# Kernel optimization log

Hardware: AMD Instinct MI355X
Metric: run time of the kernel (lower is better)

Reference implementation:

```python
import jax, jax.numpy as jnp
import numpy as np

ALPHA = 0.2  # Config.alpha, GAT default LeakyReLU slope
NUM_REL = 4
N = 4096          # num_e == batch of nodes
IN_F = 256
OUT_F = 64


def setup_inputs() -> dict:
    key = jax.random.key(0)
    k1, k2, k3, k4 = jax.random.split(key, 4)
    inp = jax.random.normal(k1, (N, IN_F), dtype=jnp.float32)
    adj = jax.random.uniform(k2, (N, N), dtype=jnp.float32)
    # xavier_uniform with gain=1.414 (sqrt(2))
    gain = 1.414
    limW = gain * np.sqrt(6.0 / (IN_F + OUT_F))
    W = jax.random.uniform(k3, (IN_F, OUT_F), minval=-limW, maxval=limW, dtype=jnp.float32)
    lima = gain * np.sqrt(6.0 / (2 * OUT_F + 1))
    a = jax.random.uniform(k4, (2 * OUT_F, 1), minval=-lima, maxval=lima, dtype=jnp.float32)
    return {"input": inp, "adj": adj, "W": W, "a": a}


def reference(input, adj, W, a):
    # h: (N, F_out)
    h = input @ W
    # The torch code builds an (N, N, 2F) concat tensor then matmuls with a.
    # Algebraically: e_ij = leakyrelu(h_i . a1 + h_j . a2) with a = [a1; a2].
    a1, a2 = a[:OUT_F], a[OUT_F:]            # (F,1) each
    s1 = (h @ a1)                            # (N,1) -> row term
    s2 = (h @ a2)                            # (N,1) -> col term
    e = jax.nn.leaky_relu(s1 + s2.T, negative_slope=ALPHA)  # (N,N)
    # attention = adj * e, replicated per relation, softmax over keys (dim 2)
    att = adj * e                            # (N,N)
    att = jnp.broadcast_to(att[None, :, :], (NUM_REL, N, N))
    att = jax.nn.softmax(att, axis=2)        # (R,N,N)
    # dropout is identity in eval mode
    h_prime = jnp.einsum('rij,jf->rif', att, h)  # (R,N,F_out)
    return jax.nn.elu(h_prime)               # concat=True -> elu
```

## Files before the change

### kernel.cpp

```cpp
#include <hip/hip_runtime.h>


#define NN 4096
#define INF 256
#define OUTF 64
#define ALPHA 0.2f
#define KCHUNKS 8
#define KCH (NN / KCHUNKS)

typedef __bf16 bf16;
typedef __bf16 bf16x4 __attribute__((ext_vector_type(4)));
typedef __bf16 bf16x8 __attribute__((ext_vector_type(8)));
typedef float floatx4 __attribute__((ext_vector_type(4)));

__global__ __launch_bounds__(256) void k_h(const float* __restrict__ input,
                                           const float* __restrict__ W,
                                           const float* __restrict__ a,
                                           bf16* __restrict__ hT,
                                           float* __restrict__ s1,
                                           float* __restrict__ s2) {
    const int wid  = threadIdx.x >> 6;
    const int lane = threadIdx.x & 63;
    const int row  = blockIdx.x * 4 + wid;
    const float* in_row = input + (size_t)row * INF;
    float acc = 0.f;
    #pragma unroll 8
    for (int k = 0; k < INF; ++k)
        acc = fmaf(in_row[k], W[k * OUTF + lane], acc);
    hT[(size_t)lane * NN + row] = (bf16)acc;
    float v1 = acc * a[lane];
    float v2 = acc * a[OUTF + lane];
    #pragma unroll
    for (int off = 32; off; off >>= 1) {
        v1 += __shfl_down(v1, off);
        v2 += __shfl_down(v2, off);
    }
    if (lane == 0) { s1[row] = v1; s2[row] = v2; }
}

__global__ __launch_bounds__(256) void k_p(const float* __restrict__ adj,
                                           const float* __restrict__ s1,
                                           const float* __restrict__ s2,
                                           bf16* __restrict__ P) {
    const int i = blockIdx.x;
    const int t = threadIdx.x;
    const int lane = t & 63, wid = t >> 6;
    const float s1i = s1[i];
    const float4* arow = (const float4*)(adj + (size_t)i * NN);
    const float4* s2v  = (const float4*)s2;
    float att[16];
    float m = -3.0e38f;
    #pragma unroll
    for (int it = 0; it < 4; ++it) {
        const int j4 = t + 256 * it;
        float4 av = arow[j4];
        float4 sv = s2v[j4];
        float e;
        e = s1i + sv.x; e = (e > 0.f ? e : ALPHA * e) * av.x; att[it*4+0] = e; m = fmaxf(m, e);
        e = s1i + sv.y; e = (e > 0.f ? e : ALPHA * e) * av.y; att[it*4+1] = e; m = fmaxf(m, e);
        e = s1i + sv.z; e = (e > 0.f ? e : ALPHA * e) * av.z; att[it*4+2] = e; m = fmaxf(m, e);
        e = s1i + sv.w; e = (e > 0.f ? e : ALPHA * e) * av.w; att[it*4+3] = e; m = fmaxf(m, e);
    }
    __shared__ float redmax[4], redsum[4];
    #pragma unroll
    for (int off = 32; off; off >>= 1) m = fmaxf(m, __shfl_xor(m, off));
    if (lane == 0) redmax[wid] = m;
    __syncthreads();
    m = fmaxf(fmaxf(redmax[0], redmax[1]), fmaxf(redmax[2], redmax[3]));
    float p[16];
    float lsum = 0.f;
    #pragma unroll
    for (int k = 0; k < 16; ++k) { p[k] = __expf(att[k] - m); lsum += p[k]; }
    #pragma unroll
    for (int off = 32; off; off >>= 1) lsum += __shfl_xor(lsum, off);
    if (lane == 0) redsum[wid] = lsum;
    __syncthreads();
    lsum = redsum[0] + redsum[1] + redsum[2] + redsum[3];
    const float rinv = 1.0f / lsum;
    bf16x4* prow = (bf16x4*)(P + (size_t)i * NN);
    #pragma unroll
    for (int it = 0; it < 4; ++it) {
        const int j4 = t + 256 * it;
        bf16x4 pv;
        pv[0] = (bf16)(p[it*4+0] * rinv);
        pv[1] = (bf16)(p[it*4+1] * rinv);
        pv[2] = (bf16)(p[it*4+2] * rinv);
        pv[3] = (bf16)(p[it*4+3] * rinv);
        prow[j4] = pv;
    }
}

__global__ __launch_bounds__(64) void k_g(const bf16* __restrict__ P,
                                          const bf16* __restrict__ hT,
                                          float* __restrict__ partial) {
    const int rg   = blockIdx.x;
    const int kc   = blockIdx.y;
    const int lane = threadIdx.x;
    const int r = lane & 15, q = lane >> 4;
    floatx4 acc[4] = {{0,0,0,0},{0,0,0,0},{0,0,0,0},{0,0,0,0}};
    const bf16* Abase = P + (size_t)(rg * 16 + r) * NN + kc * KCH + q * 8;
    const size_t hrow = (size_t)NN;
    const int kbase = kc * KCH + q * 8;
    #pragma unroll 4
    for (int s = 0; s < KCH / 32; ++s) {
        bf16x8 afrag = *(const bf16x8*)(Abase + s * 32);
        #pragma unroll
        for (int nt = 0; nt < 4; ++nt) {
            bf16x8 bfrag = *(const bf16x8*)(hT + (size_t)(nt * 16 + r) * hrow + kbase + s * 32);
            acc[nt] = __builtin_amdgcn_mfma_f32_16x16x32_bf16(afrag, bfrag, acc[nt], 0, 0, 0);
        }
    }
    float* pout = partial + (size_t)kc * (NN * OUTF);
    #pragma unroll
    for (int nt = 0; nt < 4; ++nt) {
        #pragma unroll
        for (int reg = 0; reg < 4; ++reg) {
            const int row = rg * 16 + q * 4 + reg;
            const int col = nt * 16 + r;
            pout[(size_t)row * OUTF + col] = acc[nt][reg];
        }
    }
}

__global__ __launch_bounds__(256) void k_e(const float* __restrict__ partial,
                                           float* __restrict__ out) {
    const int idx = blockIdx.x * 256 + threadIdx.x;
    float s = 0.f;
    #pragma unroll
    for (int c = 0; c < KCHUNKS; ++c) s += partial[(size_t)c * (NN * OUTF) + idx];
    const float r = s > 0.f ? s : (__expf(s) - 1.0f);
    #pragma unroll
    for (int rr = 0; rr < 4; ++rr) out[(size_t)rr * (NN * OUTF) + idx] = r;
}

extern "C" void kernel_launch(void* const* d_in, const int* in_sizes, int n_in,
                              void* d_out, int out_size, void* d_ws, size_t ws_size,
                              hipStream_t stream) {
    (void)in_sizes; (void)n_in; (void)out_size; (void)ws_size;
    const float* input = (const float*)d_in[0];
    const float* adj   = (const float*)d_in[1];
    const float* W     = (const float*)d_in[2];
    const float* a     = (const float*)d_in[3];
    float* out = (float*)d_out;

    char* ws = (char*)d_ws;
    bf16*  hT      = (bf16*)ws;
    float* s1      = (float*)(ws + (512 << 10));
    float* s2      = (float*)(ws + (528 << 10));
    bf16*  P       = (bf16*)(ws + (544 << 10));
    float* partial = (float*)(ws + (544 << 10) + (32u << 20));

    hipLaunchKernelGGL(k_h, dim3(NN / 4), dim3(256), 0, stream, input, W, a, hT, s1, s2);
    hipLaunchKernelGGL(k_p, dim3(NN), dim3(256), 0, stream, adj, s1, s2, P);
    hipLaunchKernelGGL(k_g, dim3(NN / 16, KCHUNKS), dim3(64), 0, stream, P, hT, partial);
    hipLaunchKernelGGL(k_e, dim3(NN * OUTF / 256), dim3(256), 0, stream, partial, out);
}
```

Measured before the change: 148.2 us.

## Fuse attention softmax, P@h MFMA and ELU epilogue into one kernel

```diff
diff --git a/kernel.cpp b/kernel.cpp
--- a/kernel.cpp
+++ b/kernel.cpp
@@ -5,11 +5,8 @@
 #define INF 256
 #define OUTF 64
 #define ALPHA 0.2f
-#define KCHUNKS 8
-#define KCH (NN / KCHUNKS)
 
 typedef __bf16 bf16;
-typedef __bf16 bf16x4 __attribute__((ext_vector_type(4)));
 typedef __bf16 bf16x8 __attribute__((ext_vector_type(8)));
 typedef float floatx4 __attribute__((ext_vector_type(4)));
 
@@ -38,99 +35,78 @@
     if (lane == 0) { s1[row] = v1; s2[row] = v2; }
 }
 
-__global__ __launch_bounds__(256) void k_p(const float* __restrict__ adj,
-                                           const float* __restrict__ s1,
-                                           const float* __restrict__ s2,
-                                           bf16* __restrict__ P) {
-    const int i = blockIdx.x;
-    const int t = threadIdx.x;
-    const int lane = t & 63, wid = t >> 6;
+__global__ __launch_bounds__(512, 1) void k_f(const float* __restrict__ adj,
+                                              const float* __restrict__ s1,
+                                              const float* __restrict__ s2,
+                                              const bf16* __restrict__ hT,
+                                              float* __restrict__ out) {
+    const int b    = blockIdx.x;
+    const int tid  = threadIdx.x;
+    const int w    = tid >> 6;
+    const int lane = tid & 63;
+    const int q = lane >> 4, r = lane & 15;
+    const int i = b * 16 + r;
+
     const float s1i = s1[i];
-    const float4* arow = (const float4*)(adj + (size_t)i * NN);
-    const float4* s2v  = (const float4*)s2;
-    float att[16];
-    float m = -3.0e38f;
-    #pragma unroll
-    for (int it = 0; it < 4; ++it) {
-        const int j4 = t + 256 * it;
-        float4 av = arow[j4];
-        float4 sv = s2v[j4];
-        float e;
-        e = s1i + sv.x; e = (e > 0.f ? e : ALPHA * e) * av.x; att[it*4+0] = e; m = fmaxf(m, e);
-        e = s1i + sv.y; e = (e > 0.f ? e : ALPHA * e) * av.y; att[it*4+1] = e; m = fmaxf(m, e);
-        e = s1i + sv.z; e = (e > 0.f ? e : ALPHA * e) * av.z; att[it*4+2] = e; m = fmaxf(m, e);
-        e = s1i + sv.w; e = (e > 0.f ? e : ALPHA * e) * av.w; att[it*4+3] = e; m = fmaxf(m, e);
-    }
-    __shared__ float redmax[4], redsum[4];
-    #pragma unroll
-    for (int off = 32; off; off >>= 1) m = fmaxf(m, __shfl_xor(m, off));
-    if (lane == 0) redmax[wid] = m;
-    __syncthreads();
-    m = fmaxf(fmaxf(redmax[0], redmax[1]), fmaxf(redmax[2], redmax[3]));
-    float p[16];
+    const float* arow = adj + (size_t)i * NN;
+
+    floatx4 acc[4] = {{0,0,0,0},{0,0,0,0},{0,0,0,0},{0,0,0,0}};
     float lsum = 0.f;
-    #pragma unroll
-    for (int k = 0; k < 16; ++k) { p[k] = __expf(att[k] - m); lsum += p[k]; }
-    #pragma unroll
-    for (int off = 32; off; off >>= 1) lsum += __shfl_xor(lsum, off);
-    if (lane == 0) redsum[wid] = lsum;
-    __syncthreads();
-    lsum = redsum[0] + redsum[1] + redsum[2] + redsum[3];
-    const float rinv = 1.0f / lsum;
-    bf16x4* prow = (bf16x4*)(P + (size_t)i * NN);
-    #pragma unroll
-    for (int it = 0; it < 4; ++it) {
-        const int j4 = t + 256 * it;
-        bf16x4 pv;
-        pv[0] = (bf16)(p[it*4+0] * rinv);
-        pv[1] = (bf16)(p[it*4+1] * rinv);
-        pv[2] = (bf16)(p[it*4+2] * rinv);
-        pv[3] = (bf16)(p[it*4+3] * rinv);
-        prow[j4] = pv;
-    }
-}
+    const int jw = w * 512;
 
-__global__ __launch_bounds__(64) void k_g(const bf16* __restrict__ P,
-                                          const bf16* __restrict__ hT,
-                                          float* __restrict__ partial) {
-    const int rg   = blockIdx.x;
-    const int kc   = blockIdx.y;
-    const int lane = threadIdx.x;
-    const int r = lane & 15, q = lane >> 4;
-    floatx4 acc[4] = {{0,0,0,0},{0,0,0,0},{0,0,0,0},{0,0,0,0}};
-    const bf16* Abase = P + (size_t)(rg * 16 + r) * NN + kc * KCH + q * 8;
-    const size_t hrow = (size_t)NN;
-    const int kbase = kc * KCH + q * 8;
     #pragma unroll 4
-    for (int s = 0; s < KCH / 32; ++s) {
-        bf16x8 afrag = *(const bf16x8*)(Abase + s * 32);
+    for (int t = 0; t < 16; ++t) {
+        const int jb = jw + t * 32 + q * 8;
+        const float4 a0  = *(const float4*)(arow + jb);
+        const float4 a1  = *(const float4*)(arow + jb + 4);
+        const float4 sv0 = *(const float4*)(s2 + jb);
+        const float4 sv1 = *(const float4*)(s2 + jb + 4);
+        float p0, p1, p2, p3, p4, p5, p6, p7, e;
+        e = s1i + sv0.x; e = (e > 0.f ? e : ALPHA * e) * a0.x; p0 = __expf(e);
+        e = s1i + sv0.y; e = (e > 0.f ? e : ALPHA * e) * a0.y; p1 = __expf(e);
+        e = s1i + sv0.z; e = (e > 0.f ? e : ALPHA * e) * a0.z; p2 = __expf(e);
+        e = s1i + sv0.w; e = (e > 0.f ? e : ALPHA * e) * a0.w; p3 = __expf(e);
+        e = s1i + sv1.x; e = (e > 0.f ? e : ALPHA * e) * a1.x; p4 = __expf(e);
+        e = s1i + sv1.y; e = (e > 0.f ? e : ALPHA * e) * a1.y; p5 = __expf(e);
+        e = s1i + sv1.z; e = (e > 0.f ? e : ALPHA * e) * a1.z; p6 = __expf(e);
+        e = s1i + sv1.w; e = (e > 0.f ? e : ALPHA * e) * a1.w; p7 = __expf(e);
+        lsum += ((p0 + p1) + (p2 + p3)) + ((p4 + p5) + (p6 + p7));
+        bf16x8 af;
+        af[0] = (bf16)p0; af[1] = (bf16)p1; af[2] = (bf16)p2; af[3] = (bf16)p3;
+        af[4] = (bf16)p4; af[5] = (bf16)p5; af[6] = (bf16)p6; af[7] = (bf16)p7;
         #pragma unroll
         for (int nt = 0; nt < 4; ++nt) {
-            bf16x8 bfrag = *(const bf16x8*)(hT + (size_t)(nt * 16 + r) * hrow + kbase + s * 32);
-            acc[nt] = __builtin_amdgcn_mfma_f32_16x16x32_bf16(afrag, bfrag, acc[nt], 0, 0, 0);
+            const bf16x8 bf = *(const bf16x8*)(hT + (size_t)(nt * 16 + r) * NN + jb);
+            acc[nt] = __builtin_amdgcn_mfma_f32_16x16x32_bf16(af, bf, acc[nt], 0, 0, 0);
         }
     }
-    float* pout = partial + (size_t)kc * (NN * OUTF);
+
+    lsum += __shfl_xor(lsum, 16);
+    lsum += __shfl_xor(lsum, 32);
+
+    __shared__ float sacc[8][1024];
+    __shared__ float slr[8][16];
     #pragma unroll
-    for (int nt = 0; nt < 4; ++nt) {
+    for (int nt = 0; nt < 4; ++nt)
         #pragma unroll
-        for (int reg = 0; reg < 4; ++reg) {
-            const int row = rg * 16 + q * 4 + reg;
-            const int col = nt * 16 + r;
-            pout[(size_t)row * OUTF + col] = acc[nt][reg];
-        }
+        for (int reg = 0; reg < 4; ++reg)
+            sacc[w][(q * 4 + reg) * 64 + nt * 16 + r] = acc[nt][reg];
+    if (q == 0) slr[w][r] = lsum;
+    __syncthreads();
+
+    #pragma unroll
+    for (int k = 0; k < 2; ++k) {
+        const int idx = tid + k * 512;
+        const int row = idx >> 6, f = idx & 63;
+        float s = 0.f, l = 0.f;
+        #pragma unroll
+        for (int ww = 0; ww < 8; ++ww) { s += sacc[ww][idx]; l += slr[ww][row]; }
+        float v = s / l;
+        v = v > 0.f ? v : (__expf(v) - 1.f);
+        const size_t o = (size_t)(b * 16 + row) * OUTF + f;
+        #pragma unroll
+        for (int rr = 0; rr < 4; ++rr) out[(size_t)rr * (NN * OUTF) + o] = v;
     }
-}
-
-__global__ __launch_bounds__(256) void k_e(const float* __restrict__ partial,
-                                           float* __restrict__ out) {
-    const int idx = blockIdx.x * 256 + threadIdx.x;
-    float s = 0.f;
-    #pragma unroll
-    for (int c = 0; c < KCHUNKS; ++c) s += partial[(size_t)c * (NN * OUTF) + idx];
-    const float r = s > 0.f ? s : (__expf(s) - 1.0f);
-    #pragma unroll
-    for (int rr = 0; rr < 4; ++rr) out[(size_t)rr * (NN * OUTF) + idx] = r;
 }
 
 extern "C" void kernel_launch(void* const* d_in, const int* in_sizes, int n_in,
@@ -144,14 +120,10 @@
     float* out = (float*)d_out;
 
     char* ws = (char*)d_ws;
-    bf16*  hT      = (bf16*)ws;
-    float* s1      = (float*)(ws + (512 << 10));
-    float* s2      = (float*)(ws + (528 << 10));
-    bf16*  P       = (bf16*)(ws + (544 << 10));
-    float* partial = (float*)(ws + (544 << 10) + (32u << 20));
+    bf16*  hT = (bf16*)ws;
+    float* s1 = (float*)(ws + (512 << 10));
+    float* s2 = (float*)(ws + (528 << 10));
 
     hipLaunchKernelGGL(k_h, dim3(NN / 4), dim3(256), 0, stream, input, W, a, hT, s1, s2);
-    hipLaunchKernelGGL(k_p, dim3(NN), dim3(256), 0, stream, adj, s1, s2, P);
-    hipLaunchKernelGGL(k_g, dim3(NN / 16, KCHUNKS), dim3(64), 0, stream, P, hT, partial);
-    hipLaunchKernelGGL(k_e, dim3(NN * OUTF / 256), dim3(256), 0, stream, partial, out);
+    hipLaunchKernelGGL(k_f, dim3(NN / 16), dim3(512), 0, stream, adj, s1, s2, hT, out);
 }
```

New measurement: 136.0 us. -8.3%, faster.
